# Optimization experiments

Measured on AMD Instinct MI355X. Metric: run time of the kernel, lower is better.

## Reference

```python
import jax, jax.numpy as jnp
import numpy as np

BITS = 8
CLIP_BOUND = 2.0 ** (BITS - 1) - 1.0  # 127 for int8
EPS = 1e-12


def _per_tensor_scale(x):
    # Dynamic per-tensor abs-max calibration (TensorQuantizer.update with
    # calibration over the whole tensor): scale maps abs-max to the clip bound.
    amax = jnp.max(jnp.abs(x))
    return CLIP_BOUND / jnp.maximum(amax, EPS)


def setup_inputs() -> dict:
    key = jax.random.key(0)
    k1, k2 = jax.random.split(key)
    lhs = jax.random.normal(k1, (4096, 4096), dtype=jnp.float32)
    rhs = jax.random.normal(k2, (4096, 4096), dtype=jnp.float32)
    return {"lhs": lhs, "rhs": rhs}


def reference(lhs, rhs):
    # --- calibration (scales are statistics, no gradient flows through them) ---
    ls = _per_tensor_scale(lhs)
    rs = _per_tensor_scale(rhs)

    # --- quantize to int8 grid ---
    ql = jnp.clip(jnp.round(lhs * ls), -CLIP_BOUND, CLIP_BOUND).astype(jnp.int8)
    qr = jnp.clip(jnp.round(rhs * rs), -CLIP_BOUND, CLIP_BOUND).astype(jnp.int8)

    # --- integer dot_general with int32 accumulation (aqt_dot_general core) ---
    dimension_numbers = (((1,), (0,)), ((), ()))
    acc = jax.lax.dot_general(
        ql, qr, dimension_numbers, preferred_element_type=jnp.int32
    )

    # --- dequantize by product of scales ---
    out = acc.astype(jnp.float32) / (ls * rs)
    return out
```

## Files before the change

kernel.cpp:

```cpp
#include <hip/hip_runtime.h>
#include <stdint.h>


#define NROW 4096
#define NELEM (4096 * 4096)

typedef __attribute__((ext_vector_type(4))) int int32x4;
typedef const __attribute__((address_space(1))) int8_t* gptr1_t;
typedef __attribute__((address_space(3))) int8_t* lptr3_t;

__global__ void absmax_both_kernel(const float* __restrict__ lhs,
                                   const float* __restrict__ rhs,
                                   unsigned* __restrict__ amax) {
    __shared__ float red[4];
    const int t = blockIdx.x & 1;
    const float4* x4 = (const float4*)(t ? rhs : lhs);
    const int bid = blockIdx.x >> 1;
    const int stride = (gridDim.x >> 1) * blockDim.x;
    int i = bid * blockDim.x + threadIdx.x;
    float m0 = 0.0f, m1 = 0.0f, m2 = 0.0f, m3 = 0.0f;
    for (; i + 3 * stride < NELEM / 4; i += 4 * stride) {
        float4 a = x4[i];
        float4 b = x4[i + stride];
        float4 c = x4[i + 2 * stride];
        float4 d = x4[i + 3 * stride];
        m0 = fmaxf(m0, fmaxf(fmaxf(fabsf(a.x), fabsf(a.y)),
                             fmaxf(fabsf(a.z), fabsf(a.w))));
        m1 = fmaxf(m1, fmaxf(fmaxf(fabsf(b.x), fabsf(b.y)),
                             fmaxf(fabsf(b.z), fabsf(b.w))));
        m2 = fmaxf(m2, fmaxf(fmaxf(fabsf(c.x), fabsf(c.y)),
                             fmaxf(fabsf(c.z), fabsf(c.w))));
        m3 = fmaxf(m3, fmaxf(fmaxf(fabsf(d.x), fabsf(d.y)),
                             fmaxf(fabsf(d.z), fabsf(d.w))));
    }
    for (; i < NELEM / 4; i += stride) {
        float4 a = x4[i];
        m0 = fmaxf(m0, fmaxf(fmaxf(fabsf(a.x), fabsf(a.y)),
                             fmaxf(fabsf(a.z), fabsf(a.w))));
    }
    float m = fmaxf(fmaxf(m0, m1), fmaxf(m2, m3));
    for (int off = 32; off > 0; off >>= 1)
        m = fmaxf(m, __shfl_down(m, off, 64));
    const int lane = threadIdx.x & 63, wave = threadIdx.x >> 6;
    if (lane == 0) red[wave] = m;
    __syncthreads();
    if (threadIdx.x == 0) {
        float b = fmaxf(fmaxf(red[0], red[1]), fmaxf(red[2], red[3]));
        atomicMax(amax + t, __float_as_uint(b));
    }
}

__device__ __forceinline__ int q8(float v, float s) {
    int r = __float2int_rn(v * s);
    r = r < -127 ? -127 : r;
    r = r > 127 ? 127 : r;
    return r;
}

__global__ void quant_kernel(const float* __restrict__ lhs,
                             const float* __restrict__ rhs,
                             int8_t* __restrict__ qA, int8_t* __restrict__ qT,
                             const unsigned* __restrict__ amax) {
    __shared__ int8_t sm[64][68];
    if (blockIdx.x < 16384) {
        const float s = 127.0f / fmaxf(__uint_as_float(amax[0]), 1e-12f);
        const int i = blockIdx.x * blockDim.x + threadIdx.x;
        float4 v = ((const float4*)lhs)[i];
        int b0 = q8(v.x, s), b1 = q8(v.y, s), b2 = q8(v.z, s), b3 = q8(v.w, s);
        ((int*)qA)[i] = (b0 & 0xff) | ((b1 & 0xff) << 8) | ((b2 & 0xff) << 16)
                      | ((b3 & 0xff) << 24);
    } else {
        const float s = 127.0f / fmaxf(__uint_as_float(amax[1]), 1e-12f);
        const int b = blockIdx.x - 16384;
        const int n0 = (b & 63) * 64, k0 = (b >> 6) * 64;
        const int rl = threadIdx.x >> 4;
        const int nq = threadIdx.x & 15;
        for (int r = 0; r < 4; ++r) {
            const int kl = r * 16 + rl;
            float4 v = *(const float4*)(rhs + (size_t)(k0 + kl) * NROW + n0 + nq * 4);
            sm[nq * 4 + 0][kl] = (int8_t)q8(v.x, s);
            sm[nq * 4 + 1][kl] = (int8_t)q8(v.y, s);
            sm[nq * 4 + 2][kl] = (int8_t)q8(v.z, s);
            sm[nq * 4 + 3][kl] = (int8_t)q8(v.w, s);
        }
        __syncthreads();
        const int nl = threadIdx.x >> 2;
        const int kq = threadIdx.x & 3;
        int4 w;
        w.x = *(const int*)&sm[nl][kq * 16 + 0];
        w.y = *(const int*)&sm[nl][kq * 16 + 4];
        w.z = *(const int*)&sm[nl][kq * 16 + 8];
        w.w = *(const int*)&sm[nl][kq * 16 + 12];
        *(int4*)(qT + (size_t)(n0 + nl) * NROW + k0 + kq * 16) = w;
    }
}

__global__ __launch_bounds__(256) void gemm_i8_kernel(
    const int8_t* __restrict__ qA, const int8_t* __restrict__ qBT,
    float* __restrict__ out, const unsigned* __restrict__ amax) {
    __shared__ int8_t sA[128 * 128];
    __shared__ int8_t sB[128 * 128];

    const int tid = threadIdx.x;
    const int lane = tid & 63;
    const int wave = tid >> 6;
    const int m0 = blockIdx.y * 128, n0 = blockIdx.x * 128;
    const int wm = (wave & 1) * 64;
    const int wn = (wave >> 1) * 64;

    int32x4 acc[4][4];
#pragma unroll
    for (int mi = 0; mi < 4; ++mi)
#pragma unroll
        for (int ni = 0; ni < 4; ++ni) acc[mi][ni] = (int32x4)(0);

    int rowS[4], gqS[4];
#pragma unroll
    for (int j = 0; j < 4; ++j) {
        const int c = tid + j * 256;
        rowS[j] = c >> 3;
        gqS[j] = ((c & 7) - rowS[j]) & 7;
    }

    const int q = lane >> 4;
    const int r = lane & 15;

    for (int kt = 0; kt < 32; ++kt) {
        const int kb = kt * 128;
        __syncthreads();
#pragma unroll
        for (int j = 0; j < 4; ++j) {
            const int c = tid + j * 256;
            __builtin_amdgcn_global_load_lds(
                (gptr1_t)(qA + (size_t)(m0 + rowS[j]) * NROW + kb + gqS[j] * 16),
                (lptr3_t)(sA + c * 16), 16, 0, 0);
            __builtin_amdgcn_global_load_lds(
                (gptr1_t)(qBT + (size_t)(n0 + rowS[j]) * NROW + kb + gqS[j] * 16),
                (lptr3_t)(sB + c * 16), 16, 0, 0);
        }
        __syncthreads();

#pragma unroll
        for (int kk = 0; kk < 2; ++kk) {
            int32x4 af[4], bf[4];
#pragma unroll
            for (int mi = 0; mi < 4; ++mi) {
                const int row = wm + mi * 16 + r;
                af[mi] = *(const int32x4*)(
                    sA + row * 128 + (((kk * 4 + q + row) & 7) * 16));
            }
#pragma unroll
            for (int ni = 0; ni < 4; ++ni) {
                const int row = wn + ni * 16 + r;
                bf[ni] = *(const int32x4*)(
                    sB + row * 128 + (((kk * 4 + q + row) & 7) * 16));
            }
#pragma unroll
            for (int mi = 0; mi < 4; ++mi)
#pragma unroll
                for (int ni = 0; ni < 4; ++ni)
                    acc[mi][ni] = __builtin_amdgcn_mfma_i32_16x16x64_i8(
                        af[mi], bf[ni], acc[mi][ni], 0, 0, 0);
        }
    }

    const float ls = 127.0f / fmaxf(__uint_as_float(amax[0]), 1e-12f);
    const float rs = 127.0f / fmaxf(__uint_as_float(amax[1]), 1e-12f);
    const float inv = 1.0f / (ls * rs);
#pragma unroll
    for (int mi = 0; mi < 4; ++mi)
#pragma unroll
        for (int ni = 0; ni < 4; ++ni)
#pragma unroll
            for (int reg = 0; reg < 4; ++reg) {
                const int row = m0 + wm + mi * 16 + q * 4 + reg;
                const int col = n0 + wn + ni * 16 + r;
                out[(size_t)row * NROW + col] = (float)acc[mi][ni][reg] * inv;
            }
}

extern "C" void kernel_launch(void* const* d_in, const int* in_sizes, int n_in,
                              void* d_out, int out_size, void* d_ws,
                              size_t ws_size, hipStream_t stream) {
    const float* lhs = (const float*)d_in[0];
    const float* rhs = (const float*)d_in[1];
    float* out = (float*)d_out;

    int8_t* qA = (int8_t*)d_ws;
    int8_t* qBT = qA + (size_t)16 * 1024 * 1024;
    unsigned* amax = (unsigned*)(qBT + (size_t)16 * 1024 * 1024);

    hipMemsetAsync(amax, 0, 8, stream);
    absmax_both_kernel<<<2048, 256, 0, stream>>>(lhs, rhs, amax);
    quant_kernel<<<16384 + 4096, 256, 0, stream>>>(lhs, rhs, qA, qBT, amax);
    gemm_i8_kernel<<<dim3(32, 32), 256, 0, stream>>>(qA, qBT, out, amax);
}
```

Measured before the change: 148.1 us.

## Use 256x256 GEMM tiles with triple-buffered async LDS pipeline

Restructures the int8 GEMM to 256x256 block tiles with 8 waves, a K-step of 64, and a three-stage LDS ring buffer. The next global-to-LDS loads are issued before compute, so memory latency overlaps MFMA work with one barrier per step instead of two. It also raises wave priority around the MFMA burst. In exchange it uses 96KB of LDS and more accumulator registers per thread, and the grid shrinks to 256 blocks, which may underfill the CUs.

```diff
diff --git a/kernel.cpp b/kernel.cpp
--- a/kernel.cpp
+++ b/kernel.cpp
@@ -95,86 +95,107 @@
     }
 }
 
-__global__ __launch_bounds__(256) void gemm_i8_kernel(
+__global__ __launch_bounds__(512, 2) void gemm_i8_kernel(
     const int8_t* __restrict__ qA, const int8_t* __restrict__ qBT,
     float* __restrict__ out, const unsigned* __restrict__ amax) {
-    __shared__ int8_t sA[128 * 128];
-    __shared__ int8_t sB[128 * 128];
+    __shared__ __align__(16) int8_t sA[3][256 * 64];
+    __shared__ __align__(16) int8_t sB[3][256 * 64];
 
     const int tid = threadIdx.x;
     const int lane = tid & 63;
     const int wave = tid >> 6;
-    const int m0 = blockIdx.y * 128, n0 = blockIdx.x * 128;
-    const int wm = (wave & 1) * 64;
-    const int wn = (wave >> 1) * 64;
-
-    int32x4 acc[4][4];
-#pragma unroll
-    for (int mi = 0; mi < 4; ++mi)
+    const int wm = wave >> 2;
+    const int wn = wave & 3;
+    const int m0 = blockIdx.y * 256, n0 = blockIdx.x * 256;
+
+    const int r = lane & 15;
+    const int q = lane >> 4;
+
+    const int rowA = wm * 128 + r;
+    const int aoff = rowA * 64 + ((q + (rowA >> 1)) & 3) * 16;
+    const int rowB = wn * 64 + r;
+    const int boff = rowB * 64 + ((q + (rowB >> 1)) & 3) * 16;
+
+    const int C0 = tid, C1 = tid + 512;
+    const int rS0 = C0 >> 2, G0 = ((C0 & 3) - (rS0 >> 1)) & 3;
+    const int rS1 = C1 >> 2, G1 = ((C1 & 3) - (rS1 >> 1)) & 3;
+    const gptr1_t pA0 = (gptr1_t)(qA + (size_t)(m0 + rS0) * NROW + G0 * 16);
+    const gptr1_t pA1 = (gptr1_t)(qA + (size_t)(m0 + rS1) * NROW + G1 * 16);
+    const gptr1_t pB0 = (gptr1_t)(qBT + (size_t)(n0 + rS0) * NROW + G0 * 16);
+    const gptr1_t pB1 = (gptr1_t)(qBT + (size_t)(n0 + rS1) * NROW + G1 * 16);
+    int8_t* sAf = &sA[0][0];
+    int8_t* sBf = &sB[0][0];
+    const int d0 = C0 * 16, d1 = C1 * 16;
+
+    int32x4 acc[8][4];
+#pragma unroll
+    for (int mi = 0; mi < 8; ++mi)
 #pragma unroll
         for (int ni = 0; ni < 4; ++ni) acc[mi][ni] = (int32x4)(0);
 
-    int rowS[4], gqS[4];
-#pragma unroll
-    for (int j = 0; j < 4; ++j) {
-        const int c = tid + j * 256;
-        rowS[j] = c >> 3;
-        gqS[j] = ((c & 7) - rowS[j]) & 7;
-    }
-
-    const int q = lane >> 4;
-    const int r = lane & 15;
-
-    for (int kt = 0; kt < 32; ++kt) {
-        const int kb = kt * 128;
-        __syncthreads();
-#pragma unroll
-        for (int j = 0; j < 4; ++j) {
-            const int c = tid + j * 256;
-            __builtin_amdgcn_global_load_lds(
-                (gptr1_t)(qA + (size_t)(m0 + rowS[j]) * NROW + kb + gqS[j] * 16),
-                (lptr3_t)(sA + c * 16), 16, 0, 0);
-            __builtin_amdgcn_global_load_lds(
-                (gptr1_t)(qBT + (size_t)(n0 + rowS[j]) * NROW + kb + gqS[j] * 16),
-                (lptr3_t)(sB + c * 16), 16, 0, 0);
-        }
-        __syncthreads();
-
-#pragma unroll
-        for (int kk = 0; kk < 2; ++kk) {
-            int32x4 af[4], bf[4];
-#pragma unroll
-            for (int mi = 0; mi < 4; ++mi) {
-                const int row = wm + mi * 16 + r;
-                af[mi] = *(const int32x4*)(
-                    sA + row * 128 + (((kk * 4 + q + row) & 7) * 16));
-            }
-#pragma unroll
-            for (int ni = 0; ni < 4; ++ni) {
-                const int row = wn + ni * 16 + r;
-                bf[ni] = *(const int32x4*)(
-                    sB + row * 128 + (((kk * 4 + q + row) & 7) * 16));
-            }
-#pragma unroll
-            for (int mi = 0; mi < 4; ++mi)
-#pragma unroll
-                for (int ni = 0; ni < 4; ++ni)
-                    acc[mi][ni] = __builtin_amdgcn_mfma_i32_16x16x64_i8(
-                        af[mi], bf[ni], acc[mi][ni], 0, 0, 0);
-        }
-    }
+    auto stage = [&](int buf, int kt) {
+        const int kb = kt * 64;
+        __builtin_amdgcn_global_load_lds(pA0 + kb, (lptr3_t)(sAf + buf * 16384 + d0), 16, 0, 0);
+        __builtin_amdgcn_global_load_lds(pA1 + kb, (lptr3_t)(sAf + buf * 16384 + d1), 16, 0, 0);
+        __builtin_amdgcn_global_load_lds(pB0 + kb, (lptr3_t)(sBf + buf * 16384 + d0), 16, 0, 0);
+        __builtin_amdgcn_global_load_lds(pB1 + kb, (lptr3_t)(sBf + buf * 16384 + d1), 16, 0, 0);
+    };
+
+    auto compute = [&](int cur) {
+        const int8_t* a = sAf + cur * 16384;
+        const int8_t* b = sBf + cur * 16384;
+        int32x4 af[8], bf[4];
+#pragma unroll
+        for (int mi = 0; mi < 8; ++mi)
+            af[mi] = *(const int32x4*)(a + aoff + mi * 1024);
+#pragma unroll
+        for (int ni = 0; ni < 4; ++ni)
+            bf[ni] = *(const int32x4*)(b + boff + ni * 1024);
+        __builtin_amdgcn_s_setprio(1);
+#pragma unroll
+        for (int mi = 0; mi < 8; ++mi)
+#pragma unroll
+            for (int ni = 0; ni < 4; ++ni)
+                acc[mi][ni] = __builtin_amdgcn_mfma_i32_16x16x64_i8(
+                    af[mi], bf[ni], acc[mi][ni], 0, 0, 0);
+        __builtin_amdgcn_s_setprio(0);
+    };
+
+    stage(0, 0);
+    stage(1, 1);
+    asm volatile("s_waitcnt vmcnt(4)" ::: "memory");
+    __builtin_amdgcn_s_barrier();
+    __builtin_amdgcn_sched_barrier(0);
+
+    int cur = 0, stg = 2;
+#pragma unroll 1
+    for (int kt = 0; kt < 62; ++kt) {
+        stage(stg, kt + 2);
+        compute(cur);
+        asm volatile("s_waitcnt vmcnt(4)" ::: "memory");
+        __builtin_amdgcn_s_barrier();
+        __builtin_amdgcn_sched_barrier(0);
+        cur = (cur == 2) ? 0 : cur + 1;
+        stg = (stg == 2) ? 0 : stg + 1;
+    }
+    compute(cur);
+    asm volatile("s_waitcnt vmcnt(0)" ::: "memory");
+    __builtin_amdgcn_s_barrier();
+    __builtin_amdgcn_sched_barrier(0);
+    cur = (cur == 2) ? 0 : cur + 1;
+    compute(cur);
 
     const float ls = 127.0f / fmaxf(__uint_as_float(amax[0]), 1e-12f);
     const float rs = 127.0f / fmaxf(__uint_as_float(amax[1]), 1e-12f);
     const float inv = 1.0f / (ls * rs);
 #pragma unroll
-    for (int mi = 0; mi < 4; ++mi)
+    for (int mi = 0; mi < 8; ++mi)
 #pragma unroll
         for (int ni = 0; ni < 4; ++ni)
 #pragma unroll
             for (int reg = 0; reg < 4; ++reg) {
-                const int row = m0 + wm + mi * 16 + q * 4 + reg;
-                const int col = n0 + wn + ni * 16 + r;
+                const int row = m0 + wm * 128 + mi * 16 + q * 4 + reg;
+                const int col = n0 + wn * 64 + ni * 16 + r;
                 out[(size_t)row * NROW + col] = (float)acc[mi][ni][reg] * inv;
             }
 }
@@ -193,5 +214,5 @@
     hipMemsetAsync(amax, 0, 8, stream);
     absmax_both_kernel<<<2048, 256, 0, stream>>>(lhs, rhs, amax);
     quant_kernel<<<16384 + 4096, 256, 0, stream>>>(lhs, rhs, qA, qBT, amax);
-    gemm_i8_kernel<<<dim3(32, 32), 256, 0, stream>>>(qA, qBT, out, amax);
-}
+    gemm_i8_kernel<<<dim3(16, 16), 512, 0, stream>>>(qA, qBT, out, amax);
+}
```

Result: slower. 156.7 us (+5.9%).

## Enlarge GEMM tiles to 256x256 with triple-buffered LDS and register double-buffering

Applied to the files above, without the earlier changes.

Rewrites the int8 GEMM to use 256x256 block tiles with K-step 64 and a triple-buffered LDS ring filled by async global_load_lds. Fragments are double-buffered in registers so the next LDS reads overlap with the current MFMAs, with one barrier per stage. The launch drops to 256 blocks and uses a swizzled block order for L2 reuse. It aims to raise arithmetic intensity and hide load latency, at the cost of very high register use (256 accumulator VGPRs) and only 256 workgroups, which may leave compute units underfilled.

```diff
diff --git a/kernel.cpp b/kernel.cpp
--- a/kernel.cpp
+++ b/kernel.cpp
@@ -95,86 +95,130 @@
     }
 }
 
-__global__ __launch_bounds__(256) void gemm_i8_kernel(
+__device__ __forceinline__ void mfma_all(int32x4 (&acc)[8][8],
+                                         const int32x4 (&fa)[8],
+                                         const int32x4 (&fb)[8]) {
+#pragma unroll
+    for (int mi = 0; mi < 8; ++mi)
+#pragma unroll
+        for (int ni = 0; ni < 8; ++ni)
+            acc[mi][ni] = __builtin_amdgcn_mfma_i32_16x16x64_i8(
+                fa[mi], fb[ni], acc[mi][ni], 0, 0, 0);
+}
+
+__device__ __forceinline__ void read_frags(int32x4 (&fa)[8], int32x4 (&fb)[8],
+                                           const int8_t* a, const int8_t* b,
+                                           int aoff, int boff) {
+#pragma unroll
+    for (int mi = 0; mi < 8; ++mi)
+        fa[mi] = *(const int32x4*)(a + aoff + mi * 1024);
+#pragma unroll
+    for (int ni = 0; ni < 8; ++ni)
+        fb[ni] = *(const int32x4*)(b + boff + ni * 1024);
+}
+
+__global__ __launch_bounds__(256, 1) void gemm_i8_kernel(
     const int8_t* __restrict__ qA, const int8_t* __restrict__ qBT,
     float* __restrict__ out, const unsigned* __restrict__ amax) {
-    __shared__ int8_t sA[128 * 128];
-    __shared__ int8_t sB[128 * 128];
+    __shared__ __align__(16) int8_t sA[3][256 * 64];
+    __shared__ __align__(16) int8_t sB[3][256 * 64];
 
     const int tid = threadIdx.x;
     const int lane = tid & 63;
     const int wave = tid >> 6;
-    const int m0 = blockIdx.y * 128, n0 = blockIdx.x * 128;
-    const int wm = (wave & 1) * 64;
-    const int wn = (wave >> 1) * 64;
-
-    int32x4 acc[4][4];
-#pragma unroll
-    for (int mi = 0; mi < 4; ++mi)
-#pragma unroll
-        for (int ni = 0; ni < 4; ++ni) acc[mi][ni] = (int32x4)(0);
-
-    int rowS[4], gqS[4];
+    const int wm = wave >> 1;
+    const int wn = wave & 1;
+
+    const int bid = blockIdx.y * 16 + blockIdx.x;
+    const int swz = (bid & 7) * 32 + (bid >> 3);
+    const int m0 = (swz >> 4) * 256, n0 = (swz & 15) * 256;
+
+    const int r = lane & 15;
+    const int q = lane >> 4;
+
+    const int rowA = wm * 128 + r;
+    const int aoff = rowA * 64 + ((q + (rowA >> 1)) & 3) * 16;
+    const int rowB = wn * 128 + r;
+    const int boff = rowB * 64 + ((q + (rowB >> 1)) & 3) * 16;
+
+    gptr1_t pA[4], pB[4];
 #pragma unroll
     for (int j = 0; j < 4; ++j) {
         const int c = tid + j * 256;
-        rowS[j] = c >> 3;
-        gqS[j] = ((c & 7) - rowS[j]) & 7;
-    }
-
-    const int q = lane >> 4;
-    const int r = lane & 15;
-
-    for (int kt = 0; kt < 32; ++kt) {
-        const int kb = kt * 128;
-        __syncthreads();
+        const int row = c >> 2;
+        const int G = ((c & 3) - (row >> 1)) & 3;
+        pA[j] = (gptr1_t)(qA + (size_t)(m0 + row) * NROW + G * 16);
+        pB[j] = (gptr1_t)(qBT + (size_t)(n0 + row) * NROW + G * 16);
+    }
+    int8_t* sAf = &sA[0][0];
+    int8_t* sBf = &sB[0][0];
+    const int dst0 = tid * 16;
+
+    auto stage = [&](int slot, int kb) {
 #pragma unroll
         for (int j = 0; j < 4; ++j) {
-            const int c = tid + j * 256;
             __builtin_amdgcn_global_load_lds(
-                (gptr1_t)(qA + (size_t)(m0 + rowS[j]) * NROW + kb + gqS[j] * 16),
-                (lptr3_t)(sA + c * 16), 16, 0, 0);
+                pA[j] + kb, (lptr3_t)(sAf + slot * 16384 + dst0 + j * 4096),
+                16, 0, 0);
             __builtin_amdgcn_global_load_lds(
-                (gptr1_t)(qBT + (size_t)(n0 + rowS[j]) * NROW + kb + gqS[j] * 16),
-                (lptr3_t)(sB + c * 16), 16, 0, 0);
+                pB[j] + kb, (lptr3_t)(sBf + slot * 16384 + dst0 + j * 4096),
+                16, 0, 0);
         }
-        __syncthreads();
-
-#pragma unroll
-        for (int kk = 0; kk < 2; ++kk) {
-            int32x4 af[4], bf[4];
-#pragma unroll
-            for (int mi = 0; mi < 4; ++mi) {
-                const int row = wm + mi * 16 + r;
-                af[mi] = *(const int32x4*)(
-                    sA + row * 128 + (((kk * 4 + q + row) & 7) * 16));
-            }
-#pragma unroll
-            for (int ni = 0; ni < 4; ++ni) {
-                const int row = wn + ni * 16 + r;
-                bf[ni] = *(const int32x4*)(
-                    sB + row * 128 + (((kk * 4 + q + row) & 7) * 16));
-            }
-#pragma unroll
-            for (int mi = 0; mi < 4; ++mi)
-#pragma unroll
-                for (int ni = 0; ni < 4; ++ni)
-                    acc[mi][ni] = __builtin_amdgcn_mfma_i32_16x16x64_i8(
-                        af[mi], bf[ni], acc[mi][ni], 0, 0, 0);
-        }
-    }
+    };
+
+    int32x4 acc[8][8];
+#pragma unroll
+    for (int mi = 0; mi < 8; ++mi)
+#pragma unroll
+        for (int ni = 0; ni < 8; ++ni) acc[mi][ni] = (int32x4)(0);
+
+    int32x4 fa0[8], fb0[8], fa1[8], fb1[8];
+
+    stage(0, 0);
+    stage(1, 64);
+    asm volatile("s_waitcnt vmcnt(8)" ::: "memory");
+    __builtin_amdgcn_s_barrier();
+    asm volatile("" ::: "memory");
+    read_frags(fa0, fb0, sAf, sBf, aoff, boff);
+
+    int rs = 1, ss = 2;
+#pragma unroll 1
+    for (int w = 0; w < 62; w += 2) {
+        stage(ss, (w + 2) * 64);
+        asm volatile("s_waitcnt vmcnt(8)" ::: "memory");
+        __builtin_amdgcn_s_barrier();
+        asm volatile("" ::: "memory");
+        mfma_all(acc, fa0, fb0);
+        read_frags(fa1, fb1, sAf + rs * 16384, sBf + rs * 16384, aoff, boff);
+        rs = (rs == 2) ? 0 : rs + 1;
+        ss = (ss == 2) ? 0 : ss + 1;
+        stage(ss, (w + 3) * 64);
+        asm volatile("s_waitcnt vmcnt(8)" ::: "memory");
+        __builtin_amdgcn_s_barrier();
+        asm volatile("" ::: "memory");
+        mfma_all(acc, fa1, fb1);
+        read_frags(fa0, fb0, sAf + rs * 16384, sBf + rs * 16384, aoff, boff);
+        rs = (rs == 2) ? 0 : rs + 1;
+        ss = (ss == 2) ? 0 : ss + 1;
+    }
+    asm volatile("s_waitcnt vmcnt(0)" ::: "memory");
+    __builtin_amdgcn_s_barrier();
+    asm volatile("" ::: "memory");
+    mfma_all(acc, fa0, fb0);
+    read_frags(fa1, fb1, sAf + rs * 16384, sBf + rs * 16384, aoff, boff);
+    mfma_all(acc, fa1, fb1);
 
     const float ls = 127.0f / fmaxf(__uint_as_float(amax[0]), 1e-12f);
-    const float rs = 127.0f / fmaxf(__uint_as_float(amax[1]), 1e-12f);
-    const float inv = 1.0f / (ls * rs);
-#pragma unroll
-    for (int mi = 0; mi < 4; ++mi)
-#pragma unroll
-        for (int ni = 0; ni < 4; ++ni)
+    const float rrs = 127.0f / fmaxf(__uint_as_float(amax[1]), 1e-12f);
+    const float inv = 1.0f / (ls * rrs);
+#pragma unroll
+    for (int mi = 0; mi < 8; ++mi)
+#pragma unroll
+        for (int ni = 0; ni < 8; ++ni)
 #pragma unroll
             for (int reg = 0; reg < 4; ++reg) {
-                const int row = m0 + wm + mi * 16 + q * 4 + reg;
-                const int col = n0 + wn + ni * 16 + r;
+                const int row = m0 + wm * 128 + mi * 16 + q * 4 + reg;
+                const int col = n0 + wn * 128 + ni * 16 + r;
                 out[(size_t)row * NROW + col] = (float)acc[mi][ni][reg] * inv;
             }
 }
@@ -193,5 +237,5 @@
     hipMemsetAsync(amax, 0, 8, stream);
     absmax_both_kernel<<<2048, 256, 0, stream>>>(lhs, rhs, amax);
     quant_kernel<<<16384 + 4096, 256, 0, stream>>>(lhs, rhs, qA, qBT, amax);
-    gemm_i8_kernel<<<dim3(32, 32), 256, 0, stream>>>(qA, qBT, out, amax);
-}
+    gemm_i8_kernel<<<dim3(16, 16), 256, 0, stream>>>(qA, qBT, out, amax);
+}
```

Result: slower. 438.6 us, median of 2 (+196.3%).
